# Kernel tuning notes

Measured on AMD Instinct MI355X. Metric: run time of the kernel, lower is better.

## Reference

```python
import jax, jax.numpy as jnp
import numpy as np

B, T, H = 4, 1024, 4096
N_Q, N_KV, HD = 32, 8, 128
N_REP = N_Q // N_KV
THETA = 10000.0


def setup_inputs() -> dict:
    key = jax.random.key(0)
    k0, k1, k2 = jax.random.split(key, 3)
    x = jax.random.normal(k0, (B, T, H), dtype=jnp.float32)
    w_qkv = jax.random.normal(k1, ((N_Q + 2 * N_KV) * HD, H), dtype=jnp.float32) * 0.02
    w_proj = jax.random.normal(k2, (N_Q * HD, H), dtype=jnp.float32).T * 0.02  # [H, N_Q*HD] -> stored as [out,in]=[4096,4096]
    # real RoPE frequencies, matching precompute_freqs_cis(theta=10000)
    inv_freq = 1.0 / (THETA ** (np.arange(0, HD, 2, dtype=np.float32) / HD))  # [HD/2]
    angles = np.arange(T, dtype=np.float32)[:, None] * inv_freq[None, :]      # [T, HD/2]
    freqs_cos = jnp.asarray(np.cos(angles))
    freqs_sin = jnp.asarray(np.sin(angles))
    return {"x": x, "w_qkv": w_qkv, "w_proj": w_proj,
            "freqs_cos": freqs_cos, "freqs_sin": freqs_sin}


def _rope(x, cos, sin):
    # x: [B, T, nH, HD]; consecutive pairs (x[2i], x[2i+1]) form complex numbers
    x0 = x[..., 0::2]
    x1 = x[..., 1::2]
    c = cos[None, :, None, :]
    s = sin[None, :, None, :]
    r0 = x0 * c - x1 * s
    r1 = x0 * s + x1 * c
    return jnp.stack([r0, r1], axis=-1).reshape(x.shape)


def reference(x, w_qkv, w_proj, freqs_cos, freqs_sin):
    q_per_kv = N_Q // N_KV
    qkv = jnp.einsum('bth,oh->bto', x, w_qkv)                 # [B,T,(N_Q+2*N_KV)*HD]
    qkv = qkv.reshape(B, T, N_KV, q_per_kv + 2, HD)           # interleaved GQA layout
    q = qkv[:, :, :, :q_per_kv, :].reshape(B, T, N_Q, HD)
    k = qkv[:, :, :, q_per_kv, :]                              # [B,T,N_KV,HD]
    v = qkv[:, :, :, q_per_kv + 1, :]
    q = _rope(q, freqs_cos, freqs_sin)
    k = _rope(k, freqs_cos, freqs_sin)
    k = jnp.repeat(k, N_REP, axis=2)                           # [B,T,N_Q,HD]
    v = jnp.repeat(v, N_REP, axis=2)
    q = q.transpose(0, 2, 1, 3)                                # [B,H,T,HD]
    k = k.transpose(0, 2, 1, 3)
    v = v.transpose(0, 2, 1, 3)
    scale = 1.0 / jnp.sqrt(jnp.float32(HD))
    scores = jnp.einsum('bhqd,bhkd->bhqk', q, k) * scale       # [B,H,T,T]
    causal = jnp.tril(jnp.ones((T, T), dtype=bool))
    scores = jnp.where(causal[None, None], scores, jnp.finfo(scores.dtype).min)
    attn = jax.nn.softmax(scores, axis=-1)
    out = jnp.einsum('bhqk,bhkd->bhqd', attn, v)               # [B,H,T,HD]
    out = out.transpose(0, 2, 1, 3).reshape(B, T, N_Q * HD)
    return jnp.einsum('bto,ho->bth', out, w_proj)              # RowParallel proj, [B,T,H]
```

## Files before the change

kernel.cpp:

```cpp
#include <hip/hip_runtime.h>
#include <cstddef>

#define DEVINL __device__ __forceinline__

typedef float f32x4 __attribute__((ext_vector_type(4)));
typedef __bf16 bf16x8 __attribute__((ext_vector_type(8)));

DEVINL unsigned short f2bf(float f) {
  union { float f; unsigned int u; } v; v.f = f;
  unsigned int u = v.u;
  unsigned int r = (u + 0x7fffu + ((u >> 16) & 1u)) >> 16;
  return (unsigned short)r;
}
DEVINL float bf2f(unsigned short s) {
  union { unsigned int u; float f; } v; v.u = ((unsigned int)s) << 16;
  return v.f;
}
DEVINL uint4 pack8(const unsigned short o[8]) {
  uint4 r;
  r.x = (unsigned int)o[0] | ((unsigned int)o[1] << 16);
  r.y = (unsigned int)o[2] | ((unsigned int)o[3] << 16);
  r.z = (unsigned int)o[4] | ((unsigned int)o[5] << 16);
  r.w = (unsigned int)o[6] | ((unsigned int)o[7] << 16);
  return r;
}
DEVINL void gload16(const void* g, void* l) {
  __builtin_amdgcn_global_load_lds(
      (__attribute__((address_space(1))) void*)g,
      (__attribute__((address_space(3))) void*)l, 16, 0, 0);
}

__global__ __launch_bounds__(256) void k_cvt(const float* __restrict__ in,
                                             unsigned short* __restrict__ out, int n4) {
  int i = blockIdx.x * 256 + threadIdx.x;
  if (i >= n4) return;
  float4 v = ((const float4*)in)[i];
  ushort4 o;
  o.x = f2bf(v.x); o.y = f2bf(v.y); o.z = f2bf(v.z); o.w = f2bf(v.w);
  ((ushort4*)out)[i] = o;
}

template <int OUT_BF16>
__global__ __launch_bounds__(512, 1) void k_gemm256(const unsigned short* __restrict__ A,
                                                    const unsigned short* __restrict__ Bt,
                                                    void* __restrict__ Cout,
                                                    int M, int N, int K) {
  __shared__ __align__(16) unsigned short As[2][2][256 * 32];
  __shared__ __align__(16) unsigned short Bs[2][2][256 * 32];
  const int t = threadIdx.x, lane = t & 63;
  const int wid = t >> 6, wm = wid >> 2, wn = wid & 3;
  const int fr = lane & 15, kq = lane >> 4;
  const int nwg = gridDim.x * gridDim.y;
  int lin = blockIdx.y * gridDim.x + blockIdx.x;
  lin = (lin & 7) * (nwg >> 3) + (lin >> 3);
  const int bx = lin % gridDim.x, by = lin / gridDim.x;
  const int row0 = by * 256, col0 = bx * 256;
  const int NT = K >> 6;

  int srow[2], sgs[2];
#pragma unroll
  for (int i = 0; i < 2; ++i) {
    const int off = (i * 512 + t) * 16;
    srow[i] = off >> 6;
    sgs[i] = (((off >> 4) & 3) - (srow[i] >> 1)) & 3;
  }

#define STAGE_A(KT, KS)                                                        \
  do {                                                                         \
    const int b_ = (KT) & 1;                                                   \
    _Pragma("unroll") for (int i = 0; i < 2; ++i)                              \
        gload16(A + (size_t)(row0 + srow[i]) * K + (KT) * 64 + (KS) * 32 +     \
                    sgs[i] * 8,                                                \
                (char*)&As[b_][KS][0] + i * 8192 + wid * 1024);                \
  } while (0)
#define STAGE_B(KT, KS)                                                        \
  do {                                                                         \
    const int b_ = (KT) & 1;                                                   \
    _Pragma("unroll") for (int i = 0; i < 2; ++i)                              \
        gload16(Bt + (size_t)(col0 + srow[i]) * K + (KT) * 64 + (KS) * 32 +    \
                    sgs[i] * 8,                                                \
                (char*)&Bs[b_][KS][0] + i * 8192 + wid * 1024);                \
  } while (0)
#define LDFRAG(BUFP, ROW) \
  (*(const bf16x8*)((const char*)(BUFP) + (ROW) * 64 + ((((ROW) >> 1) + kq & 3) << 4)))

  f32x4 acc[8][4];
#pragma unroll
  for (int m = 0; m < 8; ++m)
#pragma unroll
    for (int n = 0; n < 4; ++n) acc[m][n] = f32x4{0.f, 0.f, 0.f, 0.f};

  STAGE_A(0, 0); STAGE_B(0, 0); STAGE_A(0, 1); STAGE_B(0, 1);
  STAGE_A(1, 0); STAGE_B(1, 0);
  asm volatile("s_waitcnt vmcnt(8)" ::: "memory");
  __builtin_amdgcn_s_barrier();

  for (int kt = 0; kt < NT; ++kt) {
    const unsigned short* As0 = &As[kt & 1][0][0];
    const unsigned short* As1 = &As[kt & 1][1][0];
    const unsigned short* Bs0 = &Bs[kt & 1][0][0];
    const unsigned short* Bs1 = &Bs[kt & 1][1][0];
    bf16x8 a0[4], a1[4], b0[4], b1[4];

#pragma unroll
    for (int m = 0; m < 4; ++m) a0[m] = LDFRAG(As0, wm * 128 + m * 16 + fr);
#pragma unroll
    for (int n = 0; n < 4; ++n) b0[n] = LDFRAG(Bs0, wn * 64 + n * 16 + fr);
    if (kt + 1 < NT) STAGE_A(kt + 1, 1);
    __builtin_amdgcn_sched_barrier(0);
    __builtin_amdgcn_s_barrier();
    asm volatile("s_waitcnt lgkmcnt(0)" ::: "memory");
    __builtin_amdgcn_sched_barrier(0);
    __builtin_amdgcn_s_setprio(1);
#pragma unroll
    for (int m = 0; m < 4; ++m)
#pragma unroll
      for (int n = 0; n < 4; ++n)
        acc[m][n] = __builtin_amdgcn_mfma_f32_16x16x32_bf16(a0[m], b0[n], acc[m][n], 0, 0, 0);
    __builtin_amdgcn_s_setprio(0);
    __builtin_amdgcn_s_barrier();

#pragma unroll
    for (int m = 0; m < 4; ++m) a1[m] = LDFRAG(As0, wm * 128 + 64 + m * 16 + fr);
    if (kt + 1 < NT) STAGE_B(kt + 1, 1);
    __builtin_amdgcn_sched_barrier(0);
    __builtin_amdgcn_s_barrier();
    asm volatile("s_waitcnt lgkmcnt(0)" ::: "memory");
    __builtin_amdgcn_sched_barrier(0);
    __builtin_amdgcn_s_setprio(1);
#pragma unroll
    for (int m = 0; m < 4; ++m)
#pragma unroll
      for (int n = 0; n < 4; ++n)
        acc[m + 4][n] = __builtin_amdgcn_mfma_f32_16x16x32_bf16(a1[m], b0[n], acc[m + 4][n], 0, 0, 0);
    __builtin_amdgcn_s_setprio(0);
    if (kt + 1 < NT) asm volatile("s_waitcnt vmcnt(8)" ::: "memory");
    else             asm volatile("s_waitcnt vmcnt(0)" ::: "memory");
    __builtin_amdgcn_sched_barrier(0);
    __builtin_amdgcn_s_barrier();

#pragma unroll
    for (int m = 0; m < 4; ++m) a0[m] = LDFRAG(As1, wm * 128 + m * 16 + fr);
#pragma unroll
    for (int n = 0; n < 4; ++n) b1[n] = LDFRAG(Bs1, wn * 64 + n * 16 + fr);
    if (kt + 2 < NT) STAGE_A(kt + 2, 0);
    __builtin_amdgcn_sched_barrier(0);
    __builtin_amdgcn_s_barrier();
    asm volatile("s_waitcnt lgkmcnt(0)" ::: "memory");
    __builtin_amdgcn_sched_barrier(0);
    __builtin_amdgcn_s_setprio(1);
#pragma unroll
    for (int m = 0; m < 4; ++m)
#pragma unroll
      for (int n = 0; n < 4; ++n)
        acc[m][n] = __builtin_amdgcn_mfma_f32_16x16x32_bf16(a0[m], b1[n], acc[m][n], 0, 0, 0);
    __builtin_amdgcn_s_setprio(0);
    __builtin_amdgcn_s_barrier();

#pragma unroll
    for (int m = 0; m < 4; ++m) a1[m] = LDFRAG(As1, wm * 128 + 64 + m * 16 + fr);
    if (kt + 2 < NT) STAGE_B(kt + 2, 0);
    __builtin_amdgcn_sched_barrier(0);
    __builtin_amdgcn_s_barrier();
    asm volatile("s_waitcnt lgkmcnt(0)" ::: "memory");
    __builtin_amdgcn_sched_barrier(0);
    __builtin_amdgcn_s_setprio(1);
#pragma unroll
    for (int m = 0; m < 4; ++m)
#pragma unroll
      for (int n = 0; n < 4; ++n)
        acc[m + 4][n] = __builtin_amdgcn_mfma_f32_16x16x32_bf16(a1[m], b1[n], acc[m + 4][n], 0, 0, 0);
    __builtin_amdgcn_s_setprio(0);
    if (kt + 2 < NT)      asm volatile("s_waitcnt vmcnt(8)" ::: "memory");
    else if (kt + 1 < NT) asm volatile("s_waitcnt vmcnt(4)" ::: "memory");
    __builtin_amdgcn_sched_barrier(0);
    __builtin_amdgcn_s_barrier();
  }
#undef STAGE_A
#undef STAGE_B
#undef LDFRAG

  const int rsub = kq * 4;
#pragma unroll
  for (int m = 0; m < 8; ++m)
#pragma unroll
    for (int n = 0; n < 4; ++n)
#pragma unroll
      for (int r = 0; r < 4; ++r) {
        const size_t row = (size_t)row0 + wm * 128 + m * 16 + rsub + r;
        const size_t col = (size_t)col0 + wn * 64 + n * 16 + fr;
        if (OUT_BF16)
          ((unsigned short*)Cout)[row * N + col] = f2bf(acc[m][n][r]);
        else
          ((float*)Cout)[row * N + col] = acc[m][n][r];
      }
}

__global__ __launch_bounds__(256) void k_rope(const unsigned short* __restrict__ qkv,
                                              const float* __restrict__ fcos,
                                              const float* __restrict__ fsin,
                                              unsigned short* __restrict__ Qb,
                                              unsigned short* __restrict__ Kb) {
  const int idx = blockIdx.x * 256 + threadIdx.x;
  if (idx >= 4096 * 640) return;
  const int bt = idx / 640;
  const int r = idx - bt * 640;
  const int g = r / 80;
  const int rr = r - g * 80;
  const int slot = rr >> 4;
  const int d0 = (rr & 15) * 8;
  const int o0 = g * 768 + slot * 128 + d0;
  const int b = bt >> 10, tt = bt & 1023;

  uint4 raw = *(const uint4*)&qkv[(size_t)bt * 6144 + o0];
  unsigned short us[8] = {
      (unsigned short)(raw.x & 0xffff), (unsigned short)(raw.x >> 16),
      (unsigned short)(raw.y & 0xffff), (unsigned short)(raw.y >> 16),
      (unsigned short)(raw.z & 0xffff), (unsigned short)(raw.z >> 16),
      (unsigned short)(raw.w & 0xffff), (unsigned short)(raw.w >> 16)};

  float4 c = *(const float4*)&fcos[tt * 64 + (d0 >> 1)];
  float4 s = *(const float4*)&fsin[tt * 64 + (d0 >> 1)];
  const float sc = (slot < 4) ? 0.08838834764831845f : 1.0f;
  float cj[4] = {c.x, c.y, c.z, c.w};
  float sj[4] = {s.x, s.y, s.z, s.w};
  unsigned short os[8];
#pragma unroll
  for (int j = 0; j < 4; ++j) {
    float x0 = bf2f(us[2 * j]), x1 = bf2f(us[2 * j + 1]);
    os[2 * j] = f2bf((x0 * cj[j] - x1 * sj[j]) * sc);
    os[2 * j + 1] = f2bf((x0 * sj[j] + x1 * cj[j]) * sc);
  }
  if (slot < 4) {
    const int h = g * 4 + slot;
    *(uint4*)&Qb[((size_t)(b * 32 + h) * 1024 + tt) * 128 + d0] = pack8(os);
  } else {
    *(uint4*)&Kb[((size_t)(b * 8 + g) * 1024 + tt) * 128 + d0] = pack8(os);
  }
}

__global__ __launch_bounds__(256) void k_vtrans(const unsigned short* __restrict__ qkv,
                                                unsigned short* __restrict__ VT) {
  const int t = threadIdx.x;
  const int tt0 = blockIdx.x * 128;
  const int bg = blockIdx.y;
  const int b = bg >> 3, g = bg & 7;
  const int tj = t & 15;
  const int ti = t >> 4;
  union U4 { uint4 v; unsigned int u[4]; };
  U4 in[8], out[8];
  const unsigned short* src =
      qkv + (size_t)(b * 1024 + tt0 + ti * 8) * 6144 + g * 768 + 640 + tj * 8;
#pragma unroll
  for (int r = 0; r < 8; ++r) in[r].v = *(const uint4*)(src + (size_t)r * 6144);
#pragma unroll
  for (int c = 0; c < 8; ++c) {
    const unsigned int sel = (c & 1) ? 0x07060302u : 0x05040100u;
    const int dw = c >> 1;
#pragma unroll
    for (int w = 0; w < 4; ++w)
      out[c].u[w] = __builtin_amdgcn_perm(in[2 * w + 1].u[dw], in[2 * w].u[dw], sel);
  }
  unsigned short* dst = VT + (size_t)bg * 131072 + (size_t)(tj * 8) * 1024 + tt0 + ti * 8;
#pragma unroll
  for (int c = 0; c < 8; ++c) *(uint4*)(dst + (size_t)c * 1024) = out[c].v;
}

__global__ __launch_bounds__(512, 1) void k_attn(const unsigned short* __restrict__ Qb,
                                                 const unsigned short* __restrict__ Kb,
                                                 const unsigned short* __restrict__ VT,
                                                 unsigned short* __restrict__ AO) {
  __shared__ __align__(16) unsigned short Ks[2][64 * 128];
  __shared__ __align__(16) unsigned short Vt[2][128 * 64];
  __shared__ __align__(16) unsigned short Ps[8][32 * 64];
  const int t = threadIdx.x, lane = t & 63, wid = t >> 6;
  const int hh = wid >> 1, qh = wid & 1;
  const int bg = blockIdx.x, b = bg >> 3, g = bg & 7;
  const int qi = 15 - (int)blockIdx.y;
  const int q0 = qi * 64;
  const int h = g * 4 + hh;
  const int fr = lane & 15, kq = lane >> 4;
  const size_t kvbase = (size_t)bg * (1024 * 128);
  const size_t vtbase = (size_t)bg * (128 * 1024);

#define ASTAGE(TILE, BUF)                                                      \
  do {                                                                         \
    const int kv0_ = (TILE) * 64;                                              \
    _Pragma("unroll") for (int it = 0; it < 2; ++it) {                         \
      const int off = it * 8192 + t * 16;                                      \
      const int r_ = off >> 8, cb_ = off & 255;                                \
      const int scb_ = cb_ ^ ((r_ & 7) << 4);                                  \
      gload16(Kb + kvbase + (size_t)(kv0_ + r_) * 128 + (scb_ >> 1),           \
              (char*)Ks[BUF] + off);                                           \
    }                                                                          \
    _Pragma("unroll") for (int it = 0; it < 2; ++it) {                         \
      const int off = it * 8192 + t * 16;                                      \
      const int rd_ = off >> 7, cb_ = off & 127;                               \
      const int scb_ = cb_ ^ ((rd_ & 7) << 4);                                 \
      gload16(VT + vtbase + (size_t)rd_ * 1024 + kv0_ + (scb_ >> 1),           \
              (char*)Vt[BUF] + off);                                           \
    }                                                                          \
  } while (0)

  bf16x8 qf[2][4];
  {
    const unsigned short* Qp0 = Qb + ((size_t)(b * 32 + h) * 1024 + q0 + qh * 32) * 128;
#pragma unroll
    for (int qr = 0; qr < 2; ++qr)
#pragma unroll
      for (int ks = 0; ks < 4; ++ks)
        qf[qr][ks] = *(const bf16x8*)&Qp0[(size_t)(qr * 16 + fr) * 128 + ks * 32 + kq * 8];
  }
  float mrow[2][4], lrow[2][4];
#pragma unroll
  for (int qr = 0; qr < 2; ++qr)
#pragma unroll
    for (int rg = 0; rg < 4; ++rg) { mrow[qr][rg] = -1e30f; lrow[qr][rg] = 0.f; }
  f32x4 of[2][8];
#pragma unroll
  for (int qr = 0; qr < 2; ++qr)
#pragma unroll
    for (int n = 0; n < 8; ++n) of[qr][n] = f32x4{0.f, 0.f, 0.f, 0.f};

  const int ntiles = qi + 1;
  ASTAGE(0, 0);

  for (int kt = 0; kt < ntiles; ++kt) {
    const int buf = kt & 1;
    const int kv0 = kt * 64;
    if (kt + 1 < ntiles) {
      ASTAGE(kt + 1, buf ^ 1);
      asm volatile("s_waitcnt vmcnt(4)" ::: "memory");
    } else {
      asm volatile("s_waitcnt vmcnt(0)" ::: "memory");
    }
    __builtin_amdgcn_s_barrier();
    __builtin_amdgcn_sched_barrier(0);

    f32x4 sacc[2][4];
#pragma unroll
    for (int qr = 0; qr < 2; ++qr)
#pragma unroll
      for (int n = 0; n < 4; ++n) sacc[qr][n] = f32x4{0.f, 0.f, 0.f, 0.f};
#pragma unroll
    for (int n = 0; n < 4; ++n) {
      const int row = n * 16 + fr;
      const int sw = (row & 7) << 4;
      bf16x8 kf[4];
#pragma unroll
      for (int ks = 0; ks < 4; ++ks)
        kf[ks] = *(const bf16x8*)((const char*)Ks[buf] + row * 256 + ((ks * 64 + kq * 16) ^ sw));
      __builtin_amdgcn_s_setprio(1);
#pragma unroll
      for (int qr = 0; qr < 2; ++qr)
#pragma unroll
        for (int ks = 0; ks < 4; ++ks)
          sacc[qr][n] =
              __builtin_amdgcn_mfma_f32_16x16x32_bf16(qf[qr][ks], kf[ks], sacc[qr][n], 0, 0, 0);
      __builtin_amdgcn_s_setprio(0);
    }

#pragma unroll
    for (int qr = 0; qr < 2; ++qr)
#pragma unroll
      for (int rg = 0; rg < 4; ++rg) {
        const int qrow = q0 + qh * 32 + qr * 16 + kq * 4 + rg;
        float s[4];
#pragma unroll
        for (int n = 0; n < 4; ++n) {
          s[n] = sacc[qr][n][rg];
          if (kv0 + n * 16 + fr > qrow) s[n] = -1e30f;
        }
        float mx = fmaxf(fmaxf(s[0], s[1]), fmaxf(s[2], s[3]));
#pragma unroll
        for (int o = 1; o < 16; o <<= 1) mx = fmaxf(mx, __shfl_xor(mx, o));
        const float mnew = fmaxf(mrow[qr][rg], mx);
        float p[4];
#pragma unroll
        for (int n = 0; n < 4; ++n) p[n] = __expf(s[n] - mnew);
        float sum = (p[0] + p[1]) + (p[2] + p[3]);
#pragma unroll
        for (int o = 1; o < 16; o <<= 1) sum += __shfl_xor(sum, o);
        const float fac = __expf(mrow[qr][rg] - mnew);
        lrow[qr][rg] = lrow[qr][rg] * fac + sum;
        mrow[qr][rg] = mnew;
#pragma unroll
        for (int n = 0; n < 8; ++n) of[qr][n][rg] *= fac;
        const int q = qr * 16 + kq * 4 + rg;
        const int swp = (q & 7) << 4;
#pragma unroll
        for (int n = 0; n < 4; ++n)
          *(unsigned short*)((char*)Ps[wid] + q * 128 + ((2 * (n * 16 + fr)) ^ swp)) =
              f2bf(p[n]);
      }
    asm volatile("s_waitcnt lgkmcnt(0)" ::: "memory");
    __builtin_amdgcn_sched_barrier(0);

    bf16x8 pa[2][2];
#pragma unroll
    for (int qr = 0; qr < 2; ++qr) {
      const int prow = qr * 16 + fr;
      const int swp = (prow & 7) << 4;
#pragma unroll
      for (int kk = 0; kk < 2; ++kk)
        pa[qr][kk] = *(const bf16x8*)((const char*)Ps[wid] + prow * 128 +
                                      ((kk * 64 + kq * 16) ^ swp));
    }
#pragma unroll
    for (int n = 0; n < 8; ++n) {
      const int row = n * 16 + fr;
      const int sw = (row & 7) << 4;
      bf16x8 vf[2];
#pragma unroll
      for (int kk = 0; kk < 2; ++kk)
        vf[kk] = *(const bf16x8*)((const char*)Vt[buf] + row * 128 + ((kk * 64 + kq * 16) ^ sw));
      __builtin_amdgcn_s_setprio(1);
#pragma unroll
      for (int qr = 0; qr < 2; ++qr)
#pragma unroll
        for (int kk = 0; kk < 2; ++kk)
          of[qr][n] = __builtin_amdgcn_mfma_f32_16x16x32_bf16(pa[qr][kk], vf[kk], of[qr][n], 0, 0, 0);
      __builtin_amdgcn_s_setprio(0);
    }
    asm volatile("s_waitcnt lgkmcnt(0)" ::: "memory");
    __builtin_amdgcn_sched_barrier(0);
    __builtin_amdgcn_s_barrier();
  }
#undef ASTAGE

  float inv[2][4];
#pragma unroll
  for (int qr = 0; qr < 2; ++qr)
#pragma unroll
    for (int rg = 0; rg < 4; ++rg) inv[qr][rg] = 1.0f / lrow[qr][rg];
#pragma unroll
  for (int qr = 0; qr < 2; ++qr)
#pragma unroll
    for (int n = 0; n < 8; ++n)
#pragma unroll
      for (int rg = 0; rg < 4; ++rg) {
        const size_t row = (size_t)b * 1024 + q0 + qh * 32 + qr * 16 + kq * 4 + rg;
        const size_t col = (size_t)h * 128 + n * 16 + fr;
        AO[row * 4096 + col] = f2bf(of[qr][n][rg] * inv[qr][rg]);
      }
}

extern "C" void kernel_launch(void* const* d_in, const int* in_sizes, int n_in,
                              void* d_out, int out_size, void* d_ws, size_t ws_size,
                              hipStream_t stream) {
  const float* x = (const float*)d_in[0];
  const float* w_qkv = (const float*)d_in[1];
  const float* w_proj = (const float*)d_in[2];
  const float* fcos = (const float*)d_in[3];
  const float* fsin = (const float*)d_in[4];
  float* out = (float*)d_out;

  char* ws = (char*)d_ws;
  unsigned short* XB    = (unsigned short*)(ws + 0);
  unsigned short* WQKVB = (unsigned short*)(ws + 33554432);
  unsigned short* QKVB  = (unsigned short*)(ws + 83886080);
  unsigned short* QB    = (unsigned short*)(ws + 134217728);
  unsigned short* KB    = (unsigned short*)(ws + 167772160);
  unsigned short* VTB   = (unsigned short*)(ws + 176160768);
  unsigned short* WPROJB = XB;
  unsigned short* AOB    = QKVB;

  k_cvt<<<16384, 256, 0, stream>>>(x, XB, 4194304);
  k_cvt<<<24576, 256, 0, stream>>>(w_qkv, WQKVB, 6291456);
  k_gemm256<1><<<dim3(24, 16), 512, 0, stream>>>(XB, WQKVB, QKVB, 4096, 6144, 4096);
  k_cvt<<<16384, 256, 0, stream>>>(w_proj, WPROJB, 4194304);
  k_rope<<<10240, 256, 0, stream>>>(QKVB, fcos, fsin, QB, KB);
  k_vtrans<<<dim3(8, 32), 256, 0, stream>>>(QKVB, VTB);
  k_attn<<<dim3(32, 16), 512, 0, stream>>>(QB, KB, VTB, AOB);
  k_gemm256<0><<<dim3(16, 16), 512, 0, stream>>>(AOB, WPROJB, out, 4096, 4096, 4096);
}
```

Baseline: 512.3 us.

## Fuse RoPE into QKV GEMM epilogue, relax waitcnts, lazy softmax rescale

Measured after the change: 553.7 us. 1.08x slower.

```diff
diff --git a/kernel.cpp b/kernel.cpp
--- a/kernel.cpp
+++ b/kernel.cpp
@@ -40,11 +40,15 @@
   ((ushort4*)out)[i] = o;
 }
 
-template <int OUT_BF16>
+template <int MODE>
 __global__ __launch_bounds__(512, 1) void k_gemm256(const unsigned short* __restrict__ A,
                                                     const unsigned short* __restrict__ Bt,
                                                     void* __restrict__ Cout,
-                                                    int M, int N, int K) {
+                                                    int M, int N, int K,
+                                                    const float* __restrict__ fcos,
+                                                    const float* __restrict__ fsin,
+                                                    unsigned short* __restrict__ Qb,
+                                                    unsigned short* __restrict__ Kb) {
   __shared__ __align__(16) unsigned short As[2][2][256 * 32];
   __shared__ __align__(16) unsigned short Bs[2][2][256 * 32];
   const int t = threadIdx.x, lane = t & 63;
@@ -92,7 +96,7 @@
 
   STAGE_A(0, 0); STAGE_B(0, 0); STAGE_A(0, 1); STAGE_B(0, 1);
   STAGE_A(1, 0); STAGE_B(1, 0);
-  asm volatile("s_waitcnt vmcnt(8)" ::: "memory");
+  asm volatile("s_waitcnt vmcnt(4)" ::: "memory");
   __builtin_amdgcn_s_barrier();
 
   for (int kt = 0; kt < NT; ++kt) {
@@ -134,9 +138,6 @@
       for (int n = 0; n < 4; ++n)
         acc[m + 4][n] = __builtin_amdgcn_mfma_f32_16x16x32_bf16(a1[m], b0[n], acc[m + 4][n], 0, 0, 0);
     __builtin_amdgcn_s_setprio(0);
-    if (kt + 1 < NT) asm volatile("s_waitcnt vmcnt(8)" ::: "memory");
-    else             asm volatile("s_waitcnt vmcnt(0)" ::: "memory");
-    __builtin_amdgcn_sched_barrier(0);
     __builtin_amdgcn_s_barrier();
 
 #pragma unroll
@@ -159,6 +160,10 @@
 
 #pragma unroll
     for (int m = 0; m < 4; ++m) a1[m] = LDFRAG(As1, wm * 128 + 64 + m * 16 + fr);
+    if (kt + 1 < NT) {
+      if (kt + 2 < NT) asm volatile("s_waitcnt vmcnt(2)" ::: "memory");
+      else             asm volatile("s_waitcnt vmcnt(0)" ::: "memory");
+    }
     if (kt + 2 < NT) STAGE_B(kt + 2, 0);
     __builtin_amdgcn_sched_barrier(0);
     __builtin_amdgcn_s_barrier();
@@ -171,9 +176,6 @@
       for (int n = 0; n < 4; ++n)
         acc[m + 4][n] = __builtin_amdgcn_mfma_f32_16x16x32_bf16(a1[m], b1[n], acc[m + 4][n], 0, 0, 0);
     __builtin_amdgcn_s_setprio(0);
-    if (kt + 2 < NT)      asm volatile("s_waitcnt vmcnt(8)" ::: "memory");
-    else if (kt + 1 < NT) asm volatile("s_waitcnt vmcnt(4)" ::: "memory");
-    __builtin_amdgcn_sched_barrier(0);
     __builtin_amdgcn_s_barrier();
   }
 #undef STAGE_A
@@ -189,54 +191,34 @@
       for (int r = 0; r < 4; ++r) {
         const size_t row = (size_t)row0 + wm * 128 + m * 16 + rsub + r;
         const size_t col = (size_t)col0 + wn * 64 + n * 16 + fr;
-        if (OUT_BF16)
+        if constexpr (MODE == 2) {
+          const float val = acc[m][n][r];
+          const float part = __shfl_xor(val, 1);
+          const int o = (int)col;
+          const int g = o / 768;
+          const int rem = o - g * 768;
+          const int slot = rem >> 7;
+          const int d = rem & 127;
+          const int tt = (int)row & 1023, bb = (int)row >> 10;
+          if (slot == 5) {
+            ((unsigned short*)Cout)[row * N + col] = f2bf(val);
+          } else {
+            const float c = fcos[tt * 64 + (d >> 1)];
+            const float s = fsin[tt * 64 + (d >> 1)];
+            float res = (d & 1) ? (part * s + val * c) : (val * c - part * s);
+            if (slot < 4) {
+              res *= 0.08838834764831845f;
+              Qb[((size_t)(bb * 32 + g * 4 + slot) * 1024 + tt) * 128 + d] = f2bf(res);
+            } else {
+              Kb[((size_t)(bb * 8 + g) * 1024 + tt) * 128 + d] = f2bf(res);
+            }
+          }
+        } else if constexpr (MODE == 1) {
           ((unsigned short*)Cout)[row * N + col] = f2bf(acc[m][n][r]);
-        else
+        } else {
           ((float*)Cout)[row * N + col] = acc[m][n][r];
+        }
       }
-}
-
-__global__ __launch_bounds__(256) void k_rope(const unsigned short* __restrict__ qkv,
-                                              const float* __restrict__ fcos,
-                                              const float* __restrict__ fsin,
-                                              unsigned short* __restrict__ Qb,
-                                              unsigned short* __restrict__ Kb) {
-  const int idx = blockIdx.x * 256 + threadIdx.x;
-  if (idx >= 4096 * 640) return;
-  const int bt = idx / 640;
-  const int r = idx - bt * 640;
-  const int g = r / 80;
-  const int rr = r - g * 80;
-  const int slot = rr >> 4;
-  const int d0 = (rr & 15) * 8;
-  const int o0 = g * 768 + slot * 128 + d0;
-  const int b = bt >> 10, tt = bt & 1023;
-
-  uint4 raw = *(const uint4*)&qkv[(size_t)bt * 6144 + o0];
-  unsigned short us[8] = {
-      (unsigned short)(raw.x & 0xffff), (unsigned short)(raw.x >> 16),
-      (unsigned short)(raw.y & 0xffff), (unsigned short)(raw.y >> 16),
-      (unsigned short)(raw.z & 0xffff), (unsigned short)(raw.z >> 16),
-      (unsigned short)(raw.w & 0xffff), (unsigned short)(raw.w >> 16)};
-
-  float4 c = *(const float4*)&fcos[tt * 64 + (d0 >> 1)];
-  float4 s = *(const float4*)&fsin[tt * 64 + (d0 >> 1)];
-  const float sc = (slot < 4) ? 0.08838834764831845f : 1.0f;
-  float cj[4] = {c.x, c.y, c.z, c.w};
-  float sj[4] = {s.x, s.y, s.z, s.w};
-  unsigned short os[8];
-#pragma unroll
-  for (int j = 0; j < 4; ++j) {
-    float x0 = bf2f(us[2 * j]), x1 = bf2f(us[2 * j + 1]);
-    os[2 * j] = f2bf((x0 * cj[j] - x1 * sj[j]) * sc);
-    os[2 * j + 1] = f2bf((x0 * sj[j] + x1 * cj[j]) * sc);
-  }
-  if (slot < 4) {
-    const int h = g * 4 + slot;
-    *(uint4*)&Qb[((size_t)(b * 32 + h) * 1024 + tt) * 128 + d0] = pack8(os);
-  } else {
-    *(uint4*)&Kb[((size_t)(b * 8 + g) * 1024 + tt) * 128 + d0] = pack8(os);
-  }
 }
 
 __global__ __launch_bounds__(256) void k_vtrans(const unsigned short* __restrict__ qkv,
@@ -374,18 +356,21 @@
         float mx = fmaxf(fmaxf(s[0], s[1]), fmaxf(s[2], s[3]));
 #pragma unroll
         for (int o = 1; o < 16; o <<= 1) mx = fmaxf(mx, __shfl_xor(mx, o));
-        const float mnew = fmaxf(mrow[qr][rg], mx);
+        if (mx > mrow[qr][rg] + 8.f) {
+          const float fac = __expf(mrow[qr][rg] - mx);
+          lrow[qr][rg] *= fac;
+#pragma unroll
+          for (int n = 0; n < 8; ++n) of[qr][n][rg] *= fac;
+          mrow[qr][rg] = mx;
+        }
+        const float mcur = mrow[qr][rg];
         float p[4];
 #pragma unroll
-        for (int n = 0; n < 4; ++n) p[n] = __expf(s[n] - mnew);
+        for (int n = 0; n < 4; ++n) p[n] = __expf(s[n] - mcur);
         float sum = (p[0] + p[1]) + (p[2] + p[3]);
 #pragma unroll
         for (int o = 1; o < 16; o <<= 1) sum += __shfl_xor(sum, o);
-        const float fac = __expf(mrow[qr][rg] - mnew);
-        lrow[qr][rg] = lrow[qr][rg] * fac + sum;
-        mrow[qr][rg] = mnew;
-#pragma unroll
-        for (int n = 0; n < 8; ++n) of[qr][n][rg] *= fac;
+        lrow[qr][rg] += sum;
         const int q = qr * 16 + kq * 4 + rg;
         const int swp = (q & 7) << 4;
 #pragma unroll
@@ -467,10 +452,11 @@
 
   k_cvt<<<16384, 256, 0, stream>>>(x, XB, 4194304);
   k_cvt<<<24576, 256, 0, stream>>>(w_qkv, WQKVB, 6291456);
-  k_gemm256<1><<<dim3(24, 16), 512, 0, stream>>>(XB, WQKVB, QKVB, 4096, 6144, 4096);
+  k_gemm256<2><<<dim3(24, 16), 512, 0, stream>>>(XB, WQKVB, QKVB, 4096, 6144, 4096,
+                                                 fcos, fsin, QB, KB);
   k_cvt<<<16384, 256, 0, stream>>>(w_proj, WPROJB, 4194304);
-  k_rope<<<10240, 256, 0, stream>>>(QKVB, fcos, fsin, QB, KB);
   k_vtrans<<<dim3(8, 32), 256, 0, stream>>>(QKVB, VTB);
   k_attn<<<dim3(32, 16), 512, 0, stream>>>(QB, KB, VTB, AOB);
-  k_gemm256<0><<<dim3(16, 16), 512, 0, stream>>>(AOB, WPROJB, out, 4096, 4096, 4096);
-}
+  k_gemm256<0><<<dim3(16, 16), 512, 0, stream>>>(AOB, WPROJB, out, 4096, 4096, 4096,
+                                                 nullptr, nullptr, nullptr, nullptr);
+}
```
